# Kernel optimization log

Measured on AMD Instinct MI355X. Metric: run time of the kernel, lower is better.

## Reference

```python
import jax, jax.numpy as jnp
import numpy as np

# Longformer-style attention: blocked sliding-window (radius W) + attention to
# the first G global tokens. Source class body was truncated, so this follows
# the canonical Longformer local+global formulation.
B, S, D = 2, 4096, 1024
H, DH = 16, 64          # num_heads, head_dim (H*DH == D)
W = 256                  # one-sided window radius == block size
G = 64                   # number of global tokens (prefix)


def setup_inputs() -> dict:
    key = jax.random.key(0)
    ks = jax.random.split(key, 5)
    x = jax.random.normal(ks[0], (B, S, D), jnp.float32)
    init = 0.02
    Wq = jax.random.normal(ks[1], (D, D), jnp.float32) * init
    Wk = jax.random.normal(ks[2], (D, D), jnp.float32) * init
    Wv = jax.random.normal(ks[3], (D, D), jnp.float32) * init
    Wo = jax.random.normal(ks[4], (D, D), jnp.float32) * init
    return {"x": x, "Wq": Wq, "Wk": Wk, "Wv": Wv, "Wo": Wo}


def _split_heads(t):
    # [B,S,D] -> [B,H,S,DH]
    return t.reshape(B, S, H, DH).transpose(0, 2, 1, 3)


def _local_mask():
    nb = S // W
    blk = jnp.arange(nb)[:, None, None]
    qi = jnp.arange(W)[None, :, None]
    kj = jnp.arange(3 * W)[None, None, :]
    i_abs = blk * W + qi                    # absolute query index
    j_abs = blk * W - W + kj                # absolute key index in 3-block strip
    return ((j_abs >= 0) & (j_abs < S) &
            (jnp.abs(j_abs - i_abs) <= W) &
            (j_abs >= G))                    # global keys handled separately


def reference(x, Wq, Wk, Wv, Wo):
    nb = S // W
    scale = 1.0 / np.sqrt(DH).astype(np.float32)
    q = _split_heads(x @ Wq)                 # [B,H,S,DH]
    k = _split_heads(x @ Wk)
    v = _split_heads(x @ Wv)

    qb = q.reshape(B, H, nb, W, DH)
    pad = ((0, 0), (0, 0), (1, 1), (0, 0), (0, 0))
    kp = jnp.pad(k.reshape(B, H, nb, W, DH), pad)
    vp = jnp.pad(v.reshape(B, H, nb, W, DH), pad)
    # 3-block strips: [B,H,nb,3W,DH]
    k3 = jnp.concatenate([kp[:, :, :-2], kp[:, :, 1:-1], kp[:, :, 2:]], axis=3)
    v3 = jnp.concatenate([vp[:, :, :-2], vp[:, :, 1:-1], vp[:, :, 2:]], axis=3)

    s_loc = jnp.einsum('bhnqd,bhnkd->bhnqk', qb, k3) * scale  # [B,H,nb,W,3W]
    s_loc = jnp.where(_local_mask()[None, None], s_loc, jnp.float32(-1e9))

    kg, vg = k[:, :, :G], v[:, :, :G]        # global prefix tokens
    s_glb = jnp.einsum('bhnqd,bhgd->bhnqg', qb, kg) * scale    # [B,H,nb,W,G]

    p = jax.nn.softmax(jnp.concatenate([s_loc, s_glb], axis=-1), axis=-1)
    p_loc, p_glb = p[..., :3 * W], p[..., 3 * W:]

    out = (jnp.einsum('bhnqk,bhnkd->bhnqd', p_loc, v3) +
           jnp.einsum('bhnqg,bhgd->bhnqd', p_glb, vg))         # [B,H,nb,W,DH]
    out = out.reshape(B, H, S, DH).transpose(0, 2, 1, 3).reshape(B, S, D)
    return out @ Wo
```

## Files before the change

kernel.cpp:

```cpp
#include <hip/hip_runtime.h>

#define BB   2
#define SS   4096
#define DD   1024
#define HH   16
#define DHH  64
#define WW   256
#define GG   64
#define NBLK 16

typedef unsigned short ushort_t;
typedef unsigned long long u64;
typedef short  s16x8 __attribute__((ext_vector_type(8)));
typedef float  f32x4 __attribute__((ext_vector_type(4)));

#define QSCALE 0.18033688011112042f

#define VMCNT(n) asm volatile("s_waitcnt vmcnt(" #n ")" ::: "memory")

__device__ __forceinline__ ushort_t f2b(float f) {
  unsigned int u = __builtin_bit_cast(unsigned int, f);
  unsigned int r = (u + 0x7fffu + ((u >> 16) & 1u)) >> 16;
  return (ushort_t)r;
}

__device__ __forceinline__ ushort_t f2b1(float f) {
  unsigned int r;
  asm("v_cvt_pk_bf16_f32 %0, %1, %2" : "=v"(r) : "v"(f), "v"(f));
  return (ushort_t)r;
}

__device__ __forceinline__ unsigned int pk2(float a, float b) {
  unsigned int r;
  asm("v_cvt_pk_bf16_f32 %0, %1, %2" : "=v"(r) : "v"(a), "v"(b));
  return r;
}

__device__ __forceinline__ float exp2f_fast(float x) {
  return __builtin_amdgcn_exp2f(x);
}

__device__ __forceinline__ void gld16(const void* g, void* l) {
  __builtin_amdgcn_global_load_lds(
      (const __attribute__((address_space(1))) void*)g,
      (__attribute__((address_space(3))) void*)l, 16, 0, 0);
}

__global__ __launch_bounds__(256) void xcast(
    const float* __restrict__ x, ushort_t* __restrict__ xb) {
  size_t i = ((size_t)blockIdx.x * 256 + threadIdx.x) * 8;
  float4 f0 = *(const float4*)&x[i];
  float4 f1 = *(const float4*)&x[i + 4];
  ushort_t t[8];
  t[0] = f2b(f0.x); t[1] = f2b(f0.y); t[2] = f2b(f0.z); t[3] = f2b(f0.w);
  t[4] = f2b(f1.x); t[5] = f2b(f1.y); t[6] = f2b(f1.z); t[7] = f2b(f1.w);
  *(uint4*)&xb[i] = *(const uint4*)t;
}

__global__ __launch_bounds__(256) void transpose_w(
    const float* __restrict__ Wq, const float* __restrict__ Wk,
    const float* __restrict__ Wv, const float* __restrict__ Wo,
    ushort_t* __restrict__ outBase) {
  const float* src = (blockIdx.z == 0) ? Wq : (blockIdx.z == 1) ? Wk
                    : (blockIdx.z == 2) ? Wv : Wo;
  ushort_t* dst = outBase + (size_t)blockIdx.z * (1024 * 1024);
  __shared__ __align__(16) ushort_t t[64][72];
  const int tid = threadIdx.x;
  const int bx = blockIdx.x * 64, by = blockIdx.y * 64;
  const int c4 = (tid & 15) * 4;
  const int r16 = tid >> 4;
  for (int rr = r16; rr < 64; rr += 16) {
    float4 f = *(const float4*)&src[(size_t)(by + rr) * 1024 + bx + c4];
    t[c4 + 0][rr] = f2b(f.x);
    t[c4 + 1][rr] = f2b(f.y);
    t[c4 + 2][rr] = f2b(f.z);
    t[c4 + 3][rr] = f2b(f.w);
  }
  __syncthreads();
  const int sr = tid >> 3;
  const int sc = (tid & 7) * 8;
  for (int rr = sr; rr < 64; rr += 32) {
    *(uint4*)&dst[(size_t)(bx + rr) * 1024 + by + sc] = *(const uint4*)&t[rr][sc];
  }
}

__global__ __launch_bounds__(512, 2) void gemm256(
    const ushort_t* __restrict__ A, const ushort_t* __restrict__ Bt,
    ushort_t* __restrict__ O0, ushort_t* __restrict__ O1,
    ushort_t* __restrict__ O2, float* __restrict__ Of, int K) {
  __shared__ __align__(16) ushort_t SH[65536];

  const int tid  = threadIdx.x;
  const int lane = tid & 63;
  const int w    = tid >> 6;
  const int quad = lane >> 4;
  const int l16  = lane & 15;
  const int wr   = w >> 2;
  const int wc   = w & 3;

  const int id  = blockIdx.x + (gridDim.x * blockIdx.y);
  const int xcd = id & 7;
  const int seq = id >> 3;
  const int nx  = (xcd << 2) + (seq & 3);
  const int ny  = seq >> 2;
  const int bm  = nx * 256;
  const int bn  = ny * 256;

  auto Aslab = [&](int buf, int kkh) -> ushort_t* {
    return &SH[(buf * 2 + kkh) * 8192];
  };
  auto Bslab = [&](int buf, int kkh) -> ushort_t* {
    return &SH[32768 + (buf * 2 + kkh) * 8192];
  };

  const int srow = tid >> 2;
  const int sch  = (tid & 3) ^ ((srow >> 1) & 3);
  const ushort_t* Ag = A + (size_t)(bm + srow) * K + sch * 8;
  const ushort_t* Bg = Bt + (size_t)(bn + srow) * K + sch * 8;

  const int chofs = ((quad ^ ((l16 >> 1) & 3)) << 3);

  auto stage = [&](ushort_t* slab, const ushort_t* g) {
    gld16(g, &slab[tid * 8]);
    gld16(g + (size_t)128 * K, &slab[4096 + tid * 8]);
  };

  f32x4 acc[8][4] = {};
  s16x8 afrag[4], bfrag[4];

  auto ldA = [&](int buf, int kkh, int i) {
    const int row = wr * 128 + i * 16 + l16;
    return *(const s16x8*)&Aslab(buf, kkh)[row * 32 + chofs];
  };
  auto ldB = [&](int buf, int kkh, int j) {
    const int row = wc * 64 + j * 16 + l16;
    return *(const s16x8*)&Bslab(buf, kkh)[row * 32 + chofs];
  };
  auto mfma16 = [&](int ih) {
    __builtin_amdgcn_s_setprio(1);
#pragma unroll
    for (int t = 0; t < 4; t++)
#pragma unroll
      for (int j = 0; j < 4; j++)
        acc[ih * 4 + t][j] = __builtin_amdgcn_mfma_f32_16x16x32_bf16(
            afrag[t], bfrag[j], acc[ih * 4 + t][j], 0, 0, 0);
    __builtin_amdgcn_s_setprio(0);
  };

  const int NT = K >> 6;

  stage(Bslab(0, 0), Bg);
  stage(Aslab(0, 0), Ag);
  stage(Bslab(0, 1), Bg + 32);
  stage(Aslab(0, 1), Ag + 32);
  VMCNT(4);
  stage(Bslab(1, 0), Bg + 64);
  stage(Aslab(1, 0), Ag + 64);
  stage(Bslab(1, 1), Bg + 96);
  VMCNT(6);
  __builtin_amdgcn_s_barrier();

#pragma unroll 1
  for (int kt = 0; kt < NT; ++kt) {
    const int buf = kt & 1;
#pragma unroll
    for (int j = 0; j < 4; j++) bfrag[j] = ldB(buf, 0, j);
#pragma unroll
    for (int t = 0; t < 4; t++) afrag[t] = ldA(buf, 0, t);
    if (kt + 1 < NT) stage(Aslab(buf ^ 1, 1), Ag + (size_t)(kt + 1) * 64 + 32);
    __builtin_amdgcn_s_barrier();
    asm volatile("s_waitcnt lgkmcnt(0)" ::: "memory");
    mfma16(0);
    __builtin_amdgcn_s_barrier();
#pragma unroll
    for (int t = 0; t < 4; t++) afrag[t] = ldA(buf, 0, 4 + t);
    if (kt + 2 < NT) stage(Bslab(buf, 0), Bg + (size_t)(kt + 2) * 64);
    __builtin_amdgcn_s_barrier();
    asm volatile("s_waitcnt lgkmcnt(0)" ::: "memory");
    mfma16(1);
    __builtin_amdgcn_s_barrier();
#pragma unroll
    for (int j = 0; j < 4; j++) bfrag[j] = ldB(buf, 1, j);
#pragma unroll
    for (int t = 0; t < 4; t++) afrag[t] = ldA(buf, 1, t);
    if (kt + 2 < NT) stage(Aslab(buf, 0), Ag + (size_t)(kt + 2) * 64);
    __builtin_amdgcn_s_barrier();
    asm volatile("s_waitcnt lgkmcnt(0)" ::: "memory");
    mfma16(0);
    __builtin_amdgcn_s_barrier();
#pragma unroll
    for (int t = 0; t < 4; t++) afrag[t] = ldA(buf, 1, 4 + t);
    if (kt + 2 < NT) {
      stage(Bslab(buf, 1), Bg + (size_t)(kt + 2) * 64 + 32);
      VMCNT(6);
    } else if (kt + 1 < NT) {
      VMCNT(0);
    }
    __builtin_amdgcn_s_barrier();
    asm volatile("s_waitcnt lgkmcnt(0)" ::: "memory");
    mfma16(1);
    __builtin_amdgcn_s_barrier();
  }

  if (bn >= 2048) {
    const int bb = bm >> 12;
    const int n1b = bn & 1023;
    const int sb  = bm & 4095;
#pragma unroll 1
    for (int p = 0; p < 2; p++) {
      __syncthreads();
      if (wr == p) {
#pragma unroll
        for (int i = 0; i < 8; i++)
#pragma unroll
          for (int j = 0; j < 4; j++)
#pragma unroll
            for (int r = 0; r < 4; r++)
              SH[(wc * 64 + j * 16 + l16) * 136 + i * 16 + quad * 4 + r] =
                  f2b(acc[i][j][r]);
      }
      __syncthreads();
#pragma unroll
      for (int it = 0; it < 8; it++) {
        const int row = it * 32 + (tid >> 4);
        const int n1 = n1b + row;
        const int dh = n1 & 63, hh = n1 >> 6;
        const int s = sb + p * 128 + (tid & 15) * 8;
        uint4 val = *(const uint4*)&SH[row * 136 + (tid & 15) * 8];
        *(uint4*)&O2[(((size_t)bb * HH + hh) * DHH + dh) * SS + s] = val;
      }
    }
  } else {
#pragma unroll
    for (int i = 0; i < 8; i++) {
#pragma unroll
      for (int j = 0; j < 4; j++) {
#pragma unroll
        for (int r = 0; r < 4; r++) {
          int m = bm + wr * 128 + i * 16 + quad * 4 + r;
          int n = bn + wc * 64 + j * 16 + l16;
          float av = acc[i][j][r];
          int n1 = n & 1023;
          int h = n1 >> 6, dh = n1 & 63;
          int b = m >> 12, s = m & 4095;
          if (n < 1024) {
            O0[(((size_t)b * HH + h) * SS + s) * DHH + dh] = f2b(av * QSCALE);
          } else {
            O1[(((size_t)b * HH + h) * SS + s) * DHH + dh] = f2b(av);
          }
        }
      }
    }
  }
}

__global__ __launch_bounds__(256, 4) void gemmk128(
    const ushort_t* __restrict__ A, const ushort_t* __restrict__ Bt,
    float* __restrict__ Of, int K) {
  __shared__ __align__(16) ushort_t As[2][128 * 32];
  __shared__ __align__(16) ushort_t Bs[2][128 * 32];

  const int tid  = threadIdx.x;
  const int lane = tid & 63;
  const int w    = tid >> 6;
  const int quad = lane >> 4;
  const int l16  = lane & 15;
  const int wr   = w >> 1;
  const int wc   = w & 1;

  const int id  = blockIdx.x + (gridDim.x * blockIdx.y);
  const int xcd = id & 7;
  const int seq = id >> 3;
  const int nx  = (xcd << 3) + (seq & 7);
  const int ny  = seq >> 3;
  const int bm  = nx * 128;
  const int bn  = ny * 128;

  const int srow = tid >> 2;
  const int sch  = (tid & 3) ^ ((srow >> 1) & 3);
  const ushort_t* Ag = A + (size_t)(bm + srow) * K + sch * 8;
  const ushort_t* Bg = Bt + (size_t)(bn + srow) * K + sch * 8;
  const int sch2 = (tid & 3) ^ (((srow + 64) >> 1) & 3);
  const ushort_t* Ag2 = A + (size_t)(bm + srow + 64) * K + sch2 * 8;
  const ushort_t* Bg2 = Bt + (size_t)(bn + srow + 64) * K + sch2 * 8;

  const int chofs = ((quad ^ ((l16 >> 1) & 3)) << 3);

  auto stage = [&](int buf, int s) {
    gld16(Ag + (size_t)s * 32, &As[buf][tid * 8]);
    gld16(Ag2 + (size_t)s * 32, &As[buf][2048 + tid * 8]);
    gld16(Bg + (size_t)s * 32, &Bs[buf][tid * 8]);
    gld16(Bg2 + (size_t)s * 32, &Bs[buf][2048 + tid * 8]);
  };

  f32x4 acc[4][4] = {};

  const int NT = K >> 5;

  stage(0, 0);
  VMCNT(0);
  __builtin_amdgcn_s_barrier();

#pragma unroll 1
  for (int s = 0; s < NT; ++s) {
    const int buf = s & 1;
    if (s + 1 < NT) {
      stage(buf ^ 1, s + 1);
      VMCNT(4);
    } else {
      VMCNT(0);
    }
    __builtin_amdgcn_s_barrier();
    s16x8 afrag[4], bfrag[4];
#pragma unroll
    for (int t = 0; t < 4; t++)
      afrag[t] = *(const s16x8*)&As[buf][(wr * 64 + t * 16 + l16) * 32 + chofs];
#pragma unroll
    for (int j = 0; j < 4; j++)
      bfrag[j] = *(const s16x8*)&Bs[buf][(wc * 64 + j * 16 + l16) * 32 + chofs];
    asm volatile("s_waitcnt lgkmcnt(0)" ::: "memory");
    __builtin_amdgcn_s_setprio(1);
#pragma unroll
    for (int t = 0; t < 4; t++)
#pragma unroll
      for (int j = 0; j < 4; j++)
        acc[t][j] = __builtin_amdgcn_mfma_f32_16x16x32_bf16(
            afrag[t], bfrag[j], acc[t][j], 0, 0, 0);
    __builtin_amdgcn_s_setprio(0);
    __builtin_amdgcn_s_barrier();
  }

#pragma unroll
  for (int i = 0; i < 4; i++) {
#pragma unroll
    for (int j = 0; j < 4; j++) {
#pragma unroll
      for (int r = 0; r < 4; r++) {
        int m = bm + wr * 64 + i * 16 + quad * 4 + r;
        int n = bn + wc * 64 + j * 16 + l16;
        Of[(size_t)m * DD + n] = acc[i][j][r];
      }
    }
  }
}

__global__ __launch_bounds__(256, 2) void attn_kernel(
    const ushort_t* __restrict__ q, const ushort_t* __restrict__ k,
    const ushort_t* __restrict__ vT, ushort_t* __restrict__ out) {
  const int blk = blockIdx.x;
  const int h   = blockIdx.y;
  const int b   = blockIdx.z;
  const int tid  = threadIdx.x;
  const int lane = tid & 63;
  const int w    = tid >> 6;
  const int quad = lane >> 4;
  const int l16  = lane & 15;
  const int l7   = l16 & 7;

  const size_t bh = ((size_t)b * HH + h) * SS * DHH;
  const ushort_t* qb  = q + bh;
  const ushort_t* kb  = k + bh;
  const ushort_t* vtb = vT + bh;

  __shared__ __align__(16) ushort_t Ps[4][64 * 64];
  ushort_t* Pw = &Ps[w][0];

  const int q0 = blk * WW + w * 64;

  const int wofs = l16 * 64 + 4 * (quad & 1);
  const int hq1  = quad >> 1;
  const int rofs = l16 * 64;

  s16x8 aq[4][2];
#pragma unroll
  for (int mt = 0; mt < 4; mt++)
#pragma unroll
    for (int x = 0; x < 2; x++)
      aq[mt][x] = *(const s16x8*)&qb[(size_t)(q0 + mt * 16 + l16) * DHH + x * 32 + quad * 8];

  f32x4 oacc[4][4] = {};
  f32x4 rsacc[4] = {};

  s16x8 vone;
#pragma unroll
  for (int j = 0; j < 8; j++) vone[j] = (short)0x3F80;

  s16x8 bk[4][2];
  s16x8 bv[4][2];

  auto LOADK = [&](int j0s) {
    const ushort_t* kc = kb + (size_t)j0s * DHH;
#pragma unroll
    for (int nt = 0; nt < 4; nt++)
#pragma unroll
      for (int x = 0; x < 2; x++)
        bk[nt][x] = *(const s16x8*)&kc[(nt * 16 + l16) * DHH + x * 32 + quad * 8];
  };
  auto LOADV = [&](int j0s) {
    const ushort_t* vc = vtb + j0s;
#pragma unroll
    for (int dt = 0; dt < 4; dt++)
#pragma unroll
      for (int x = 0; x < 2; x++)
        bv[dt][x] = *(const s16x8*)&vc[(size_t)(dt * 16 + l16) * SS + x * 32 + quad * 8];
  };

  const int jlo = (q0 - (int)WW < (int)GG) ? (int)GG : (q0 - (int)WW);
  int jhi = q0 + (int)WW;
  if (jhi > SS - 64) jhi = SS - 64;

  int j0  = jlo;
  int j0u = __builtin_amdgcn_readfirstlane(j0);
  LOADK(j0u);

  bool last = false;
  while (!last) {
    int jn = j0 + 64;
    if (j0 == 0) { last = true; jn = 0; }
    else if (jn > jhi) jn = 0;

    LOADV(j0u);

    const int dlt = j0 - q0;
    const bool needmask = (j0 != 0) && (dlt < -193 || dlt > 193);

#pragma unroll
    for (int nt = 0; nt < 4; nt++) {
      const int jbase = j0 + nt * 16 + quad * 4;
#pragma unroll
      for (int mt = 0; mt < 4; mt++) {
        f32x4 s4 = {0.f, 0.f, 0.f, 0.f};
        s4 = __builtin_amdgcn_mfma_f32_16x16x32_bf16(bk[nt][0], aq[mt][0], s4, 0, 0, 0);
        s4 = __builtin_amdgcn_mfma_f32_16x16x32_bf16(bk[nt][1], aq[mt][1], s4, 0, 0, 0);
        float p[4];
#pragma unroll
        for (int r = 0; r < 4; r++) {
          if (needmask) {
            int d = jbase + r - (q0 + mt * 16 + l16);
            p[r] = (d <= (int)WW && d >= -(int)WW) ? exp2f_fast(s4[r]) : 0.0f;
          } else {
            p[r] = exp2f_fast(s4[r]);
          }
        }
        unsigned int lo = pk2(p[0], p[1]);
        unsigned int hi = pk2(p[2], p[3]);
        u64 val = __builtin_bit_cast(u64, (uint2){lo, hi});
        const int ch = ((nt << 1) | hq1) ^ l7;
        *(u64*)&Pw[wofs + mt * 1024 + ch * 8] = val;
      }
    }

    int jnu = __builtin_amdgcn_readfirstlane(jn);
    if (!last) LOADK(jnu);

    __builtin_amdgcn_s_setprio(1);
#pragma unroll
    for (int ll = 0; ll < 64; ll += 32) {
      s16x8 ap[4];
#pragma unroll
      for (int mt = 0; mt < 4; mt++) {
        const int chR = (quad + (ll >> 3)) ^ l7;
        ap[mt] = *(const s16x8*)&Pw[rofs + mt * 1024 + chR * 8];
      }
#pragma unroll
      for (int mt = 0; mt < 4; mt++) {
        rsacc[mt] = __builtin_amdgcn_mfma_f32_16x16x32_bf16(ap[mt], vone, rsacc[mt], 0, 0, 0);
#pragma unroll
        for (int dt = 0; dt < 4; dt++)
          oacc[mt][dt] = __builtin_amdgcn_mfma_f32_16x16x32_bf16(ap[mt], bv[dt][ll >> 5], oacc[mt][dt], 0, 0, 0);
      }
    }
    __builtin_amdgcn_s_setprio(0);

    j0 = jn; j0u = jnu;
  }

#pragma unroll
  for (int mt = 0; mt < 4; mt++) {
#pragma unroll
    for (int r = 0; r < 4; r++) {
      float inv = __builtin_amdgcn_rcpf(rsacc[mt][r]);
      int srow2 = q0 + mt * 16 + quad * 4 + r;
      size_t orow = ((size_t)b * SS + srow2) * DD + h * DHH;
#pragma unroll
      for (int dt = 0; dt < 4; dt++)
        out[orow + dt * 16 + l16] = f2b1(oacc[mt][dt][r] * inv);
    }
  }
}

extern "C" void kernel_launch(void* const* d_in, const int* in_sizes, int n_in,
                              void* d_out, int out_size, void* d_ws, size_t ws_size,
                              hipStream_t stream) {
  const float *x, *Wq, *Wk, *Wv, *Wo;
  if (n_in == 5 && in_sizes[4] == 8388608) {
    Wk = (const float*)d_in[0]; Wo = (const float*)d_in[1];
    Wq = (const float*)d_in[2]; Wv = (const float*)d_in[3];
    x  = (const float*)d_in[4];
  } else {
    x  = (const float*)d_in[0]; Wq = (const float*)d_in[1];
    Wk = (const float*)d_in[2]; Wv = (const float*)d_in[3];
    Wo = (const float*)d_in[4];
  }
  float* out = (float*)d_out;

  char* ws = (char*)d_ws;
  ushort_t* wqkvT = (ushort_t*)(ws);
  ushort_t* woT   = (ushort_t*)(ws + 6291456);
  ushort_t* qbuf  = (ushort_t*)(ws + 8388608);
  ushort_t* kbuf  = (ushort_t*)(ws + 8388608 + 16777216);
  ushort_t* vbuf  = (ushort_t*)(ws + 8388608 + 2 * 16777216);
  ushort_t* attn  = (ushort_t*)(ws + 8388608 + 3 * 16777216);
  ushort_t* xb    = attn;

  xcast<<<dim3(4096), 256, 0, stream>>>(x, xb);
  transpose_w<<<dim3(16, 16, 4), 256, 0, stream>>>(Wq, Wk, Wv, Wo, wqkvT);
  gemm256<<<dim3(32, 12), 512, 0, stream>>>(xb, wqkvT, qbuf, kbuf, vbuf, nullptr, 1024);
  attn_kernel<<<dim3(NBLK, HH, BB), 256, 0, stream>>>(qbuf, kbuf, vbuf, attn);
  gemmk128<<<dim3(64, 8), 256, 0, stream>>>(attn, woT, out, 1024);
}
```

Before: 234.3 us.

## Share K/V tiles across warps via triple-buffered LDS staging

Before, each of the four warps loaded its own K and V^T chunks straight from global memory into registers. Now the whole block walks a shared list of 64-key chunks spanning the three-block strip plus the global prefix, stages each chunk into a triple-buffered LDS ring with async loads, and warps read their MFMA operands from LDS. Warps skip chunks outside their own window. This cuts redundant global traffic, roughly fourfold, but adds block-wide barriers, 48KB more LDS that may lower occupancy, and idle iterations for warps with no work in a chunk.

New measurement: 246.4 us. 5.2% more time.

```diff
diff --git a/kernel.cpp b/kernel.cpp
--- a/kernel.cpp
+++ b/kernel.cpp
@@ -362,6 +362,8 @@
   const ushort_t* kb  = k + bh;
   const ushort_t* vtb = vT + bh;
 
+  __shared__ __align__(16) ushort_t Ks[3][64 * 64];
+  __shared__ __align__(16) ushort_t Vs[3][64 * 64];
   __shared__ __align__(16) ushort_t Ps[4][64 * 64];
   ushort_t* Pw = &Ps[w][0];
 
@@ -371,6 +373,32 @@
   const int hq1  = quad >> 1;
   const int rofs = l16 * 64;
 
+  int list[13];
+  int n = 0;
+#pragma unroll
+  for (int c = 0; c < 12; c++) {
+    int j = blk * WW - WW + c * 64;
+    if (j >= GG && j < SS) list[n++] = j;
+  }
+  list[n++] = 0;
+
+  const int srow = tid >> 3;
+  const int schw = (tid & 7) ^ (srow & 7);
+  auto stageKV = [&](int buf, int j0s) {
+    const ushort_t* kc = kb + (size_t)(j0s + srow) * DHH + schw * 8;
+    const ushort_t* vc = vtb + (size_t)srow * SS + j0s + schw * 8;
+    gld16(kc,                    &Ks[buf][tid * 8]);
+    gld16(kc + (size_t)32 * DHH, &Ks[buf][2048 + tid * 8]);
+    gld16(vc,                    &Vs[buf][tid * 8]);
+    gld16(vc + (size_t)32 * SS,  &Vs[buf][2048 + tid * 8]);
+  };
+  auto ldK = [&](int buf, int nt, int x) {
+    return *(const s16x8*)&Ks[buf][(nt * 16 + l16) * 64 + (((x << 2) + quad) ^ l7) * 8];
+  };
+  auto ldV = [&](int buf, int dt, int x) {
+    return *(const s16x8*)&Vs[buf][(dt * 16 + l16) * 64 + (((x << 2) + quad) ^ l7) * 8];
+  };
+
   s16x8 aq[4][2];
 #pragma unroll
   for (int mt = 0; mt < 4; mt++)
@@ -385,53 +413,33 @@
 #pragma unroll
   for (int j = 0; j < 8; j++) vone[j] = (short)0x3F80;
 
-  s16x8 bk[4][2];
-  s16x8 bv[4][2];
-
-  auto LOADK = [&](int j0s) {
-    const ushort_t* kc = kb + (size_t)j0s * DHH;
-#pragma unroll
-    for (int nt = 0; nt < 4; nt++)
-#pragma unroll
-      for (int x = 0; x < 2; x++)
-        bk[nt][x] = *(const s16x8*)&kc[(nt * 16 + l16) * DHH + x * 32 + quad * 8];
-  };
-  auto LOADV = [&](int j0s) {
-    const ushort_t* vc = vtb + j0s;
-#pragma unroll
-    for (int dt = 0; dt < 4; dt++)
-#pragma unroll
-      for (int x = 0; x < 2; x++)
-        bv[dt][x] = *(const s16x8*)&vc[(size_t)(dt * 16 + l16) * SS + x * 32 + quad * 8];
-  };
-
-  const int jlo = (q0 - (int)WW < (int)GG) ? (int)GG : (q0 - (int)WW);
-  int jhi = q0 + (int)WW;
-  if (jhi > SS - 64) jhi = SS - 64;
-
-  int j0  = jlo;
-  int j0u = __builtin_amdgcn_readfirstlane(j0);
-  LOADK(j0u);
-
-  bool last = false;
-  while (!last) {
-    int jn = j0 + 64;
-    if (j0 == 0) { last = true; jn = 0; }
-    else if (jn > jhi) jn = 0;
-
-    LOADV(j0u);
-
+  stageKV(0, list[0]);
+  stageKV(1, list[1]);
+
+#pragma unroll 1
+  for (int i = 0; i < n; i++) {
+    if (i + 1 < n) { VMCNT(4); } else { VMCNT(0); }
+    __builtin_amdgcn_s_barrier();
+    if (i + 2 < n) stageKV((i + 2) % 3, list[i + 2]);
+
+    const int buf = i - (i / 3) * 3;
+    const int j0 = list[i];
+    const bool isglb = (i == n - 1);
     const int dlt = j0 - q0;
-    const bool needmask = (j0 != 0) && (dlt < -193 || dlt > 193);
+    const bool haswork = isglb || (dlt >= -319 && dlt <= 319);
+    if (!haswork) continue;
+    const bool needmask = !isglb && (dlt < -193 || dlt > 193);
 
 #pragma unroll
     for (int nt = 0; nt < 4; nt++) {
+      s16x8 bk0 = ldK(buf, nt, 0);
+      s16x8 bk1 = ldK(buf, nt, 1);
       const int jbase = j0 + nt * 16 + quad * 4;
 #pragma unroll
       for (int mt = 0; mt < 4; mt++) {
         f32x4 s4 = {0.f, 0.f, 0.f, 0.f};
-        s4 = __builtin_amdgcn_mfma_f32_16x16x32_bf16(bk[nt][0], aq[mt][0], s4, 0, 0, 0);
-        s4 = __builtin_amdgcn_mfma_f32_16x16x32_bf16(bk[nt][1], aq[mt][1], s4, 0, 0, 0);
+        s4 = __builtin_amdgcn_mfma_f32_16x16x32_bf16(bk0, aq[mt][0], s4, 0, 0, 0);
+        s4 = __builtin_amdgcn_mfma_f32_16x16x32_bf16(bk1, aq[mt][1], s4, 0, 0, 0);
         float p[4];
 #pragma unroll
         for (int r = 0; r < 4; r++) {
@@ -450,29 +458,26 @@
       }
     }
 
-    int jnu = __builtin_amdgcn_readfirstlane(jn);
-    if (!last) LOADK(jnu);
-
     __builtin_amdgcn_s_setprio(1);
 #pragma unroll
     for (int ll = 0; ll < 64; ll += 32) {
-      s16x8 ap[4];
+      s16x8 ap[4], bv_[4];
 #pragma unroll
       for (int mt = 0; mt < 4; mt++) {
         const int chR = (quad + (ll >> 3)) ^ l7;
         ap[mt] = *(const s16x8*)&Pw[rofs + mt * 1024 + chR * 8];
       }
 #pragma unroll
+      for (int dt = 0; dt < 4; dt++) bv_[dt] = ldV(buf, dt, ll >> 5);
+#pragma unroll
       for (int mt = 0; mt < 4; mt++) {
         rsacc[mt] = __builtin_amdgcn_mfma_f32_16x16x32_bf16(ap[mt], vone, rsacc[mt], 0, 0, 0);
 #pragma unroll
         for (int dt = 0; dt < 4; dt++)
-          oacc[mt][dt] = __builtin_amdgcn_mfma_f32_16x16x32_bf16(ap[mt], bv[dt][ll >> 5], oacc[mt][dt], 0, 0, 0);
+          oacc[mt][dt] = __builtin_amdgcn_mfma_f32_16x16x32_bf16(ap[mt], bv_[dt], oacc[mt][dt], 0, 0, 0);
       }
     }
     __builtin_amdgcn_s_setprio(0);
-
-    j0 = jn; j0u = jnu;
   }
 
 #pragma unroll
```
